# Performance work log

Hardware: AMD Instinct MI355X
Metric: run time of the kernel (lower is better)

Reference implementation:

```python
import jax, jax.numpy as jnp
import numpy as np

N = 65536      # batch of CPU-state samples
D = 64         # byte-embedding dim
H = 512        # expert hidden dim
V = 256        # byte vocabulary / result logits
NFLAGS = 8
# number of embedded inputs per expert
KS = {"alu": 4, "logic": 4, "move": 5, "flow": 6, "stack": 6}


def setup_inputs() -> dict:
    key = jax.random.key(0)
    ks = list(jax.random.split(key, 64))
    nk = lambda: ks.pop()
    rint = lambda mx: jax.random.randint(nk(), (N,), 0, mx, dtype=jnp.int32)
    inp = {n: rint(256) for n in ["A", "X", "Y", "SP", "P", "PCH", "PCL", "Op", "Val"]}
    # deterministic opcode -> functional-unit map (stand-in for build_fu_map)
    inp["fu_map"] = (jnp.arange(256, dtype=jnp.int32) % 5)
    p = lambda shape: jax.random.normal(nk(), shape, dtype=jnp.float32) * 0.02
    for name, k in KS.items():
        inp[f"{name}_emb"] = p((k, V, D))
        inp[f"{name}_W1"] = p((k * D, H))
        inp[f"{name}_b1"] = jnp.zeros((H,), jnp.float32)
    inp["alu_Wr"] = p((H, V)); inp["alu_Wf"] = p((H, NFLAGS))
    inp["logic_Wr"] = p((H, V)); inp["logic_Wf"] = p((H, NFLAGS))
    inp["move_Wo"] = p((H, V))
    inp["flow_Wo"] = p((H, V))
    inp["stack_Wo"] = p((H, V))
    return inp


def _expert_hidden(emb, idx_list, W1, b1):
    # emb: [k, 256, D]; idx_list: k arrays of [N] byte indices
    ids = jnp.stack(idx_list)                                  # [k, N]
    f = emb[jnp.arange(emb.shape[0])[:, None], ids]            # [k, N, D] gather
    f = jnp.moveaxis(f, 0, 1).reshape(ids.shape[1], -1)        # [N, k*D]
    return jax.nn.gelu(f @ W1 + b1)                            # [N, H]


def reference(A, X, Y, SP, P, PCH, PCL, Op, Val, fu_map,
              alu_emb, alu_W1, alu_b1, alu_Wr, alu_Wf,
              logic_emb, logic_W1, logic_b1, logic_Wr, logic_Wf,
              move_emb, move_W1, move_b1, move_Wo,
              flow_emb, flow_W1, flow_b1, flow_Wo,
              stack_emb, stack_W1, stack_b1, stack_Wo):
    # deterministic zero-cost router: opcode -> FU id
    fu = fu_map[Op]                                            # [N]
    carry = P & 1                                              # carry bit of status reg
    mask = lambda k: (fu == k)[:, None].astype(jnp.float32)
    # ALU (FU 0): a, operand, carry, opcode -> result + flags logits
    h = _expert_hidden(alu_emb, [A, Val, carry, Op], alu_W1, alu_b1)
    alu = jnp.concatenate([h @ alu_Wr, h @ alu_Wf], -1) * mask(0)      # [N, 264]
    # LOGIC (FU 1): same inputs, separate params
    h = _expert_hidden(logic_emb, [A, Val, carry, Op], logic_W1, logic_b1)
    logic = jnp.concatenate([h @ logic_Wr, h @ logic_Wf], -1) * mask(1)  # [N, 264]
    # MOVE (FU 2): a, x, y, operand, opcode
    move = (_expert_hidden(move_emb, [A, X, Y, Val, Op], move_W1, move_b1) @ move_Wo) * mask(2)
    # FLOW (FU 3): pc (as PCH,PCL bytes), flags, target, sp, opcode
    flow = (_expert_hidden(flow_emb, [PCH, PCL, P, Val, SP, Op], flow_W1, flow_b1) @ flow_Wo) * mask(3)
    # STACK (FU 4): a, x, sp, flags, stack_top, opcode
    stack = (_expert_hidden(stack_emb, [A, X, SP, P, Val, Op], stack_W1, stack_b1) @ stack_Wo) * mask(4)
    # dense capacity-1 dispatch: each sample's row is nonzero only in its FU's slice
    return jnp.concatenate([alu, logic, move, flow, stack], -1)        # [N, 1296]
```

## Files before the change

kernel.cpp:

```cpp
#include <hip/hip_runtime.h>

#define DEV __device__ __forceinline__

typedef __attribute__((ext_vector_type(8))) short short8;
typedef __attribute__((ext_vector_type(4))) float f32x4;
typedef unsigned short u16;

struct Ptrs { const void* p[32]; };

constexpr int N_TOK = 65536;
constexpr int cK  [5] = {4,4,5,6,6};
constexpr int cK1 [5] = {256,256,320,384,384};
constexpr int cKT [5] = {8,8,10,12,12};
constexpr int cN2 [5] = {264,264,256,256,256};
constexpr int cNT [5] = {17,17,16,16,16};
constexpr int cC0 [5] = {0,264,528,784,1040};
constexpr int cKID[5][6] = {{0,8,9,7,0,0},{0,8,9,7,0,0},{0,1,2,8,7,0},
                            {5,6,4,8,3,7},{0,1,3,4,8,7}};
constexpr int cEOFF[5] = {0,65536,131072,212992,311296};
constexpr int cWOFF[5] = {0,131072,262144,425984,622592};
constexpr int cHOFF[5] = {0,139264,278528,417792,557056};
constexpr int EMB_TOT = 409600, W1_TOT = 819200, HEAD_TOT = 696320;
constexpr int PREP_TOT = EMB_TOT + W1_TOT + HEAD_TOT;

constexpr size_t WS_COUNTS = 0;
constexpr size_t WS_BUCKET = 256;
constexpr size_t WS_EMB    = 256 + (size_t)5 * N_TOK * 4;
constexpr size_t WS_W1T    = WS_EMB + (size_t)EMB_TOT * 2;
constexpr size_t WS_HT     = WS_W1T + (size_t)W1_TOT * 2;

constexpr int ROWS = 64;
constexpr int HP   = 520;

struct Smem {
  u16 hbuf[ROWS * HP];
  int tokb[ROWS];
  int idsb[ROWS * 6];
};

DEV u16 f2bf(float f) {
  unsigned u = __builtin_bit_cast(unsigned, f);
  u += 0x7FFFu + ((u >> 16) & 1u);
  return (u16)(u >> 16);
}

DEV float gelu_f(float x) {
  float u = 0.7978845608028654f * x * (1.0f + 0.044715f * x * x);
  float t2 = fminf(fmaxf(2.0f * u, -30.0f), 30.0f);
  float e = __expf(t2);
  float th = (e - 1.0f) / (e + 1.0f);
  return 0.5f * x * (1.0f + th);
}

__global__ __launch_bounds__(256) void prep_kernel(Ptrs in, u16* embB, u16* w1tB, u16* hTB) {
  int idx = blockIdx.x * 256 + threadIdx.x;
  if (idx < EMB_TOT) {
    int e = 0, off = idx;
    while (off >= cK[e] * 16384) { off -= cK[e] * 16384; ++e; }
    const float* src = (const float*)in.p[10 + 3*e];
    embB[cEOFF[e] + off] = f2bf(src[off]);
  } else if (idx < EMB_TOT + W1_TOT) {
    int off = idx - EMB_TOT;
    int e = 0;
    while (off >= 512 * cK1[e]) { off -= 512 * cK1[e]; ++e; }
    int K1 = cK1[e];
    int n = off / K1, k = off - n * K1;
    const float* w1 = (const float*)in.p[11 + 3*e];
    w1tB[cWOFF[e] + off] = f2bf(w1[k * 512 + n]);
  } else {
    int off = idx - (EMB_TOT + W1_TOT);
    int e = off / 139264, r = off - e * 139264;
    int n = r >> 9, k = r & 511;
    float v = 0.0f;
    if (e < 2) {
      if (n < 256)       v = ((const float*)in.p[25 + 2*e])[k * 256 + n];
      else if (n < 264)  v = ((const float*)in.p[26 + 2*e])[k * 8 + (n - 256)];
    } else {
      if (n < 256)       v = ((const float*)in.p[29 + (e - 2)])[k * 256 + n];
    }
    hTB[cHOFF[e] + r] = f2bf(v);
  }
}

__global__ __launch_bounds__(256) void bucket_kernel(const int* Op, const int* fu_map,
                                                     int* counts, int* buckets) {
  __shared__ int lc[5], lb[5];
  int tid = threadIdx.x;
  if (tid < 5) lc[tid] = 0;
  __syncthreads();
  int t = blockIdx.x * 256 + tid;
  int fu = fu_map[Op[t]];
  int lp = atomicAdd(&lc[fu], 1);
  __syncthreads();
  if (tid < 5) lb[tid] = atomicAdd(&counts[tid], lc[tid]);
  __syncthreads();
  buckets[fu * N_TOK + lb[fu] + lp] = t;
}

template<int E>
DEV void expert_tile(const Ptrs& in, int tile, int count, const int* buckets,
                     const u16* embB, const u16* w1tB, const u16* hTB,
                     float* out, Smem& sm) {
  constexpr int K1 = cK1[E], KT = cKT[E], N2 = cN2[E], C0 = cC0[E];
  constexpr int NT = cNT[E], KE = cK[E];

  const int tid = threadIdx.x;
  const int vr = min(count - tile * ROWS, ROWS);
  const int rbase = E * N_TOK + tile * ROWS;

  __syncthreads();

  if (tid < ROWS)
    sm.tokb[tid] = (tid < vr) ? buckets[rbase + tid] : -1;
  for (int i = tid; i < ROWS * KE; i += 256) {
    int r = i / KE, k = i - r * KE;
    int t = buckets[rbase + ((r < vr) ? r : 0)];
    int s = cKID[E][k];
    int v = (s == 9) ? (((const int*)in.p[4])[t] & 1)
                     : ((const int*)in.p[s])[t];
    sm.idsb[r * 6 + k] = v;
  }
  __syncthreads();

  const int lane = tid & 63, wave = tid >> 6;
  const int l15 = lane & 15, lq = lane >> 4;

  {
    constexpr int ZC  = (1296 - N2) / 4;
    constexpr int ZLO = C0 / 4;
    constexpr int ZHI = (C0 + N2) / 4;
    const f32x4 z4 = {0.f, 0.f, 0.f, 0.f};
    for (int r = wave; r < vr; r += 4) {
      float* rowp = out + (size_t)sm.tokb[r] * 1296;
      #pragma unroll
      for (int c = 0; c < ZC; c += 64) {
        int cc = c + lane;
        if (cc < ZC) {
          int col4 = (cc < ZLO) ? cc : (cc - ZLO + ZHI);
          __builtin_nontemporal_store(z4, (f32x4*)(rowp + col4 * 4));
        }
      }
    }
  }

  int myids[4][KE];
  #pragma unroll
  for (int m = 0; m < 4; ++m)
    #pragma unroll
    for (int k = 0; k < KE; ++k)
      myids[m][k] = sm.idsb[(m * 16 + l15) * 6 + k];

  const u16* embE = embB + cEOFF[E];
  const u16* w1e  = w1tB + cWOFF[E];
  const float* b1 = (const float*)in.p[12 + 3 * E];

  #pragma unroll 1
  for (int half = 0; half < 2; ++half) {
    f32x4 acc[4][4];
    const f32x4 z = {0.f, 0.f, 0.f, 0.f};
    #pragma unroll
    for (int m = 0; m < 4; ++m)
      #pragma unroll
      for (int nt = 0; nt < 4; ++nt) acc[m][nt] = z;

    #pragma unroll
    for (int kt = 0; kt < KT; ++kt) {
      const int kf = kt >> 1;
      const int d  = (kt & 1) * 32 + lq * 8;
      short8 a[4];
      #pragma unroll
      for (int m = 0; m < 4; ++m)
        a[m] = *(const short8*)(embE + ((size_t)(kf * 256 + myids[m][kf]) << 6) + d);
      #pragma unroll
      for (int nt = 0; nt < 4; ++nt) {
        int n0 = wave * 128 + half * 64 + nt * 16;
        short8 b = *(const short8*)(w1e + (n0 + l15) * K1 + kt * 32 + lq * 8);
        #pragma unroll
        for (int m = 0; m < 4; ++m)
          acc[m][nt] = __builtin_amdgcn_mfma_f32_16x16x32_bf16(a[m], b, acc[m][nt], 0, 0, 0);
      }
    }
    #pragma unroll
    for (int nt = 0; nt < 4; ++nt) {
      int col = wave * 128 + half * 64 + nt * 16 + l15;
      float b1v = b1[col];
      #pragma unroll
      for (int m = 0; m < 4; ++m)
        #pragma unroll
        for (int r = 0; r < 4; ++r)
          sm.hbuf[(m * 16 + lq * 4 + r) * HP + col] = f2bf(gelu_f(acc[m][nt][r] + b1v));
    }
  }
  __syncthreads();

  const u16* hTe = hTB + cHOFF[E];
  f32x4 acc2[4][5];
  {
    const f32x4 z = {0.f, 0.f, 0.f, 0.f};
    #pragma unroll
    for (int m = 0; m < 4; ++m)
      #pragma unroll
      for (int j = 0; j < 5; ++j) acc2[m][j] = z;
  }
  #pragma unroll 4
  for (int kt = 0; kt < 16; ++kt) {
    short8 a[4];
    #pragma unroll
    for (int m = 0; m < 4; ++m)
      a[m] = *(const short8*)(sm.hbuf + (m * 16 + l15) * HP + kt * 32 + lq * 8);
    #pragma unroll
    for (int j = 0; j < 5; ++j) {
      int nt = wave + 4 * j;
      if (nt >= NT) break;
      short8 b = *(const short8*)(hTe + (nt * 16 + l15) * 512 + kt * 32 + lq * 8);
      #pragma unroll
      for (int m = 0; m < 4; ++m)
        acc2[m][j] = __builtin_amdgcn_mfma_f32_16x16x32_bf16(a[m], b, acc2[m][j], 0, 0, 0);
    }
  }

  int trow[4][4];
  #pragma unroll
  for (int m = 0; m < 4; ++m)
    #pragma unroll
    for (int r = 0; r < 4; ++r)
      trow[m][r] = sm.tokb[m * 16 + lq * 4 + r];

  #pragma unroll
  for (int j = 0; j < 5; ++j) {
    int nt = wave + 4 * j;
    if (nt >= NT) break;
    int coln = nt * 16 + l15;
    if (coln < N2) {
      #pragma unroll
      for (int m = 0; m < 4; ++m)
        #pragma unroll
        for (int r = 0; r < 4; ++r) {
          int t = trow[m][r];
          if (t >= 0)
            __builtin_nontemporal_store(acc2[m][j][r],
                                        out + (size_t)t * 1296 + C0 + coln);
        }
    }
  }
}

__global__ __launch_bounds__(256, 2) void moe_kernel(Ptrs in, const int* counts,
                                                     const int* buckets,
                                                     const u16* embB, const u16* w1tB,
                                                     const u16* hTB, float* out) {
  __shared__ Smem sm;
  int c0 = counts[0], c1 = counts[1], c2 = counts[2], c3 = counts[3], c4 = counts[4];
  int t0 = (c0 + ROWS - 1) / ROWS;
  int t1 = (c1 + ROWS - 1) / ROWS;
  int t2 = (c2 + ROWS - 1) / ROWS;
  int t3 = (c3 + ROWS - 1) / ROWS;
  int t4 = (c4 + ROWS - 1) / ROWS;
  int p1 = t0, p2 = p1 + t1, p3 = p2 + t2, p4 = p3 + t3, p5 = p4 + t4;

  const int x = blockIdx.x & 7;
  const int slot = blockIdx.x >> 3;
  const int beg = (x * p5) >> 3;
  const int end = ((x + 1) * p5) >> 3;

  for (int g = beg + slot; g < end; g += 64) {
    int e = 0, base = 0, cnt = c0;
    if (g >= p1) { e = 1; base = p1; cnt = c1; }
    if (g >= p2) { e = 2; base = p2; cnt = c2; }
    if (g >= p3) { e = 3; base = p3; cnt = c3; }
    if (g >= p4) { e = 4; base = p4; cnt = c4; }
    int tile = g - base;
    switch (e) {
      case 0: expert_tile<0>(in, tile, cnt, buckets, embB, w1tB, hTB, out, sm); break;
      case 1: expert_tile<1>(in, tile, cnt, buckets, embB, w1tB, hTB, out, sm); break;
      case 2: expert_tile<2>(in, tile, cnt, buckets, embB, w1tB, hTB, out, sm); break;
      case 3: expert_tile<3>(in, tile, cnt, buckets, embB, w1tB, hTB, out, sm); break;
      case 4: expert_tile<4>(in, tile, cnt, buckets, embB, w1tB, hTB, out, sm); break;
    }
  }
}

extern "C" void kernel_launch(void* const* d_in, const int* in_sizes, int n_in,
                              void* d_out, int out_size, void* d_ws, size_t ws_size,
                              hipStream_t stream) {
  char* ws = (char*)d_ws;
  int* counts  = (int*)(ws + WS_COUNTS);
  int* buckets = (int*)(ws + WS_BUCKET);
  u16* embB    = (u16*)(ws + WS_EMB);
  u16* w1tB    = (u16*)(ws + WS_W1T);
  u16* hTB     = (u16*)(ws + WS_HT);

  Ptrs P;
  for (int i = 0; i < 32; ++i) P.p[i] = d_in[i];

  (void)hipMemsetAsync(counts, 0, 5 * sizeof(int), stream);
  prep_kernel<<<PREP_TOT / 256, 256, 0, stream>>>(P, embB, w1tB, hTB);
  bucket_kernel<<<N_TOK / 256, 256, 0, stream>>>((const int*)d_in[7], (const int*)d_in[9],
                                                 counts, buckets);
  moe_kernel<<<512, 256, 0, stream>>>(P, counts, buckets, embB, w1tB, hTB,
                                      (float*)d_out);
}
```

Measured before the change: 282.4 us.

## Double row tile to 128 and stage gathered embeddings in swizzled LDS

Each tile now covers 128 token rows with 512 threads (8 waves) instead of 64 rows with 256. The embedding rows are gathered once into LDS with an XOR swizzle before the first GEMM, rather than each wave re-fetching them from global memory per k-step. Each wave now owns 64 hidden columns across all 128 rows, so every W1 and head weight fragment is reused over twice as many rows. In exchange it needs about 137 KB of dynamic shared memory, which likely limits each CU to one block and may require a raised dynamic-LDS limit. It also raises accumulator register pressure.

```diff
diff --git a/kernel.cpp b/kernel.cpp
--- a/kernel.cpp
+++ b/kernel.cpp
@@ -11,7 +11,6 @@
 constexpr int N_TOK = 65536;
 constexpr int cK  [5] = {4,4,5,6,6};
 constexpr int cK1 [5] = {256,256,320,384,384};
-constexpr int cKT [5] = {8,8,10,12,12};
 constexpr int cN2 [5] = {264,264,256,256,256};
 constexpr int cNT [5] = {17,17,16,16,16};
 constexpr int cC0 [5] = {0,264,528,784,1040};
@@ -29,14 +28,12 @@
 constexpr size_t WS_W1T    = WS_EMB + (size_t)EMB_TOT * 2;
 constexpr size_t WS_HT     = WS_W1T + (size_t)W1_TOT * 2;
 
-constexpr int ROWS = 64;
+constexpr int ROWS = 128;
 constexpr int HP   = 520;
 
-struct Smem {
-  u16 hbuf[ROWS * HP];
-  int tokb[ROWS];
-  int idsb[ROWS * 6];
-};
+constexpr int TOK_OFF = ROWS * HP * 2;
+constexpr int IDS_OFF = TOK_OFF + ROWS * 4;
+constexpr int LDS_BYTES = IDS_OFF + ROWS * 6 * 4;
 
 DEV u16 f2bf(float f) {
   unsigned u = __builtin_bit_cast(unsigned, f);
@@ -100,9 +97,15 @@
 template<int E>
 DEV void expert_tile(const Ptrs& in, int tile, int count, const int* buckets,
                      const u16* embB, const u16* w1tB, const u16* hTB,
-                     float* out, Smem& sm) {
-  constexpr int K1 = cK1[E], KT = cKT[E], N2 = cN2[E], C0 = cC0[E];
+                     float* out, char* smem) {
+  constexpr int K1 = cK1[E], KT = cK1[E] / 32, N2 = cN2[E], C0 = cC0[E];
   constexpr int NT = cNT[E], KE = cK[E];
+  constexpr int FB  = K1 * 2;
+  constexpr int CPR = KE * 8;
+
+  u16* hbuf = (u16*)smem;
+  int* tokb = (int*)(smem + TOK_OFF);
+  int* idsb = (int*)(smem + IDS_OFF);
 
   const int tid = threadIdx.x;
   const int vr = min(count - tile * ROWS, ROWS);
@@ -111,27 +114,27 @@
   __syncthreads();
 
   if (tid < ROWS)
-    sm.tokb[tid] = (tid < vr) ? buckets[rbase + tid] : -1;
-  for (int i = tid; i < ROWS * KE; i += 256) {
+    tokb[tid] = (tid < vr) ? buckets[rbase + tid] : -1;
+  for (int i = tid; i < ROWS * KE; i += 512) {
     int r = i / KE, k = i - r * KE;
     int t = buckets[rbase + ((r < vr) ? r : 0)];
     int s = cKID[E][k];
     int v = (s == 9) ? (((const int*)in.p[4])[t] & 1)
                      : ((const int*)in.p[s])[t];
-    sm.idsb[r * 6 + k] = v;
+    idsb[r * 6 + k] = v;
   }
   __syncthreads();
 
   const int lane = tid & 63, wave = tid >> 6;
-  const int l15 = lane & 15, lq = lane >> 4;
+  const int l15 = lane & 15, lq = (lane >> 4) & 3;
 
   {
     constexpr int ZC  = (1296 - N2) / 4;
     constexpr int ZLO = C0 / 4;
     constexpr int ZHI = (C0 + N2) / 4;
     const f32x4 z4 = {0.f, 0.f, 0.f, 0.f};
-    for (int r = wave; r < vr; r += 4) {
-      float* rowp = out + (size_t)sm.tokb[r] * 1296;
+    for (int r = wave; r < vr; r += 8) {
+      float* rowp = out + (size_t)tokb[r] * 1296;
       #pragma unroll
       for (int c = 0; c < ZC; c += 64) {
         int cc = c + lane;
@@ -143,113 +146,124 @@
     }
   }
 
-  int myids[4][KE];
-  #pragma unroll
-  for (int m = 0; m < 4; ++m)
-    #pragma unroll
-    for (int k = 0; k < KE; ++k)
-      myids[m][k] = sm.idsb[(m * 16 + l15) * 6 + k];
-
-  const u16* embE = embB + cEOFF[E];
+  {
+    const u16* embE = embB + cEOFF[E];
+    short8 val[KT];
+    int    dst[KT];
+    #pragma unroll
+    for (int it = 0; it < KT; ++it) {
+      int d = tid + it * 512;
+      int r = d / CPR, c = d - r * CPR;
+      int k = c >> 3;
+      int id = idsb[r * 6 + k];
+      val[it] = *(const short8*)(embE + (size_t)((k * 256 + id) << 6) + ((c & 7) << 3));
+      dst[it] = r * FB + ((c * 16) ^ ((r & 7) << 4));
+    }
+    #pragma unroll
+    for (int it = 0; it < KT; ++it)
+      *(short8*)(smem + dst[it]) = val[it];
+  }
+  __syncthreads();
+
   const u16* w1e  = w1tB + cWOFF[E];
   const float* b1 = (const float*)in.p[12 + 3 * E];
 
-  #pragma unroll 1
-  for (int half = 0; half < 2; ++half) {
-    f32x4 acc[4][4];
-    const f32x4 z = {0.f, 0.f, 0.f, 0.f};
-    #pragma unroll
-    for (int m = 0; m < 4; ++m)
-      #pragma unroll
-      for (int nt = 0; nt < 4; ++nt) acc[m][nt] = z;
-
-    #pragma unroll
-    for (int kt = 0; kt < KT; ++kt) {
-      const int kf = kt >> 1;
-      const int d  = (kt & 1) * 32 + lq * 8;
-      short8 a[4];
-      #pragma unroll
-      for (int m = 0; m < 4; ++m)
-        a[m] = *(const short8*)(embE + ((size_t)(kf * 256 + myids[m][kf]) << 6) + d);
-      #pragma unroll
-      for (int nt = 0; nt < 4; ++nt) {
-        int n0 = wave * 128 + half * 64 + nt * 16;
-        short8 b = *(const short8*)(w1e + (n0 + l15) * K1 + kt * 32 + lq * 8);
-        #pragma unroll
-        for (int m = 0; m < 4; ++m)
-          acc[m][nt] = __builtin_amdgcn_mfma_f32_16x16x32_bf16(a[m], b, acc[m][nt], 0, 0, 0);
-      }
-    }
-    #pragma unroll
-    for (int nt = 0; nt < 4; ++nt) {
-      int col = wave * 128 + half * 64 + nt * 16 + l15;
-      float b1v = b1[col];
-      #pragma unroll
-      for (int m = 0; m < 4; ++m)
-        #pragma unroll
-        for (int r = 0; r < 4; ++r)
-          sm.hbuf[(m * 16 + lq * 4 + r) * HP + col] = f2bf(gelu_f(acc[m][nt][r] + b1v));
-    }
-  }
-  __syncthreads();
-
-  const u16* hTe = hTB + cHOFF[E];
-  f32x4 acc2[4][5];
+  f32x4 acc[8][4];
   {
     const f32x4 z = {0.f, 0.f, 0.f, 0.f};
     #pragma unroll
-    for (int m = 0; m < 4; ++m)
-      #pragma unroll
-      for (int j = 0; j < 5; ++j) acc2[m][j] = z;
+    for (int m = 0; m < 8; ++m)
+      #pragma unroll
+      for (int nt = 0; nt < 4; ++nt) acc[m][nt] = z;
+  }
+  #pragma unroll 2
+  for (int kt = 0; kt < KT; ++kt) {
+    short8 a[8], b[4];
+    #pragma unroll
+    for (int m = 0; m < 8; ++m) {
+      int row = m * 16 + l15;
+      a[m] = *(const short8*)(smem + row * FB + ((kt * 64 + lq * 16) ^ ((row & 7) << 4)));
+    }
+    #pragma unroll
+    for (int nt = 0; nt < 4; ++nt)
+      b[nt] = *(const short8*)(w1e + (wave * 64 + nt * 16 + l15) * K1 + kt * 32 + lq * 8);
+    #pragma unroll
+    for (int nt = 0; nt < 4; ++nt)
+      #pragma unroll
+      for (int m = 0; m < 8; ++m)
+        acc[m][nt] = __builtin_amdgcn_mfma_f32_16x16x32_bf16(a[m], b[nt], acc[m][nt], 0, 0, 0);
+  }
+  __syncthreads();
+
+  #pragma unroll
+  for (int nt = 0; nt < 4; ++nt) {
+    int col = wave * 64 + nt * 16 + l15;
+    float b1v = b1[col];
+    #pragma unroll
+    for (int m = 0; m < 8; ++m)
+      #pragma unroll
+      for (int q = 0; q < 4; ++q)
+        hbuf[(m * 16 + lq * 4 + q) * HP + col] = f2bf(gelu_f(acc[m][nt][q] + b1v));
+  }
+  __syncthreads();
+
+  const u16* hTe = hTB + cHOFF[E];
+  f32x4 acc2[8][3];
+  {
+    const f32x4 z = {0.f, 0.f, 0.f, 0.f};
+    #pragma unroll
+    for (int m = 0; m < 8; ++m)
+      #pragma unroll
+      for (int j = 0; j < 3; ++j) acc2[m][j] = z;
   }
   #pragma unroll 4
   for (int kt = 0; kt < 16; ++kt) {
-    short8 a[4];
-    #pragma unroll
-    for (int m = 0; m < 4; ++m)
-      a[m] = *(const short8*)(sm.hbuf + (m * 16 + l15) * HP + kt * 32 + lq * 8);
-    #pragma unroll
-    for (int j = 0; j < 5; ++j) {
-      int nt = wave + 4 * j;
+    short8 a[8];
+    #pragma unroll
+    for (int m = 0; m < 8; ++m)
+      a[m] = *(const short8*)(hbuf + (m * 16 + l15) * HP + kt * 32 + lq * 8);
+    #pragma unroll
+    for (int j = 0; j < 3; ++j) {
+      int nt = wave + 8 * j;
       if (nt >= NT) break;
       short8 b = *(const short8*)(hTe + (nt * 16 + l15) * 512 + kt * 32 + lq * 8);
       #pragma unroll
-      for (int m = 0; m < 4; ++m)
+      for (int m = 0; m < 8; ++m)
         acc2[m][j] = __builtin_amdgcn_mfma_f32_16x16x32_bf16(a[m], b, acc2[m][j], 0, 0, 0);
     }
   }
 
-  int trow[4][4];
+  int trow[8][4];
   #pragma unroll
-  for (int m = 0; m < 4; ++m)
-    #pragma unroll
-    for (int r = 0; r < 4; ++r)
-      trow[m][r] = sm.tokb[m * 16 + lq * 4 + r];
+  for (int m = 0; m < 8; ++m)
+    #pragma unroll
+    for (int q = 0; q < 4; ++q)
+      trow[m][q] = tokb[m * 16 + lq * 4 + q];
 
   #pragma unroll
-  for (int j = 0; j < 5; ++j) {
-    int nt = wave + 4 * j;
+  for (int j = 0; j < 3; ++j) {
+    int nt = wave + 8 * j;
     if (nt >= NT) break;
     int coln = nt * 16 + l15;
     if (coln < N2) {
       #pragma unroll
-      for (int m = 0; m < 4; ++m)
+      for (int m = 0; m < 8; ++m)
         #pragma unroll
-        for (int r = 0; r < 4; ++r) {
-          int t = trow[m][r];
+        for (int q = 0; q < 4; ++q) {
+          int t = trow[m][q];
           if (t >= 0)
-            __builtin_nontemporal_store(acc2[m][j][r],
+            __builtin_nontemporal_store(acc2[m][j][q],
                                         out + (size_t)t * 1296 + C0 + coln);
         }
     }
   }
 }
 
-__global__ __launch_bounds__(256, 2) void moe_kernel(Ptrs in, const int* counts,
+__global__ __launch_bounds__(512, 2) void moe_kernel(Ptrs in, const int* counts,
                                                      const int* buckets,
                                                      const u16* embB, const u16* w1tB,
                                                      const u16* hTB, float* out) {
-  __shared__ Smem sm;
+  extern __shared__ char smem[];
   int c0 = counts[0], c1 = counts[1], c2 = counts[2], c3 = counts[3], c4 = counts[4];
   int t0 = (c0 + ROWS - 1) / ROWS;
   int t1 = (c1 + ROWS - 1) / ROWS;
@@ -271,11 +285,11 @@
     if (g >= p4) { e = 4; base = p4; cnt = c4; }
     int tile = g - base;
     switch (e) {
-      case 0: expert_tile<0>(in, tile, cnt, buckets, embB, w1tB, hTB, out, sm); break;
-      case 1: expert_tile<1>(in, tile, cnt, buckets, embB, w1tB, hTB, out, sm); break;
-      case 2: expert_tile<2>(in, tile, cnt, buckets, embB, w1tB, hTB, out, sm); break;
-      case 3: expert_tile<3>(in, tile, cnt, buckets, embB, w1tB, hTB, out, sm); break;
-      case 4: expert_tile<4>(in, tile, cnt, buckets, embB, w1tB, hTB, out, sm); break;
+      case 0: expert_tile<0>(in, tile, cnt, buckets, embB, w1tB, hTB, out, smem); break;
+      case 1: expert_tile<1>(in, tile, cnt, buckets, embB, w1tB, hTB, out, smem); break;
+      case 2: expert_tile<2>(in, tile, cnt, buckets, embB, w1tB, hTB, out, smem); break;
+      case 3: expert_tile<3>(in, tile, cnt, buckets, embB, w1tB, hTB, out, smem); break;
+      case 4: expert_tile<4>(in, tile, cnt, buckets, embB, w1tB, hTB, out, smem); break;
     }
   }
 }
@@ -297,6 +311,6 @@
   prep_kernel<<<PREP_TOT / 256, 256, 0, stream>>>(P, embB, w1tB, hTB);
   bucket_kernel<<<N_TOK / 256, 256, 0, stream>>>((const int*)d_in[7], (const int*)d_in[9],
                                                  counts, buckets);
-  moe_kernel<<<512, 256, 0, stream>>>(P, counts, buckets, embB, w1tB, hTB,
-                                      (float*)d_out);
-}
+  moe_kernel<<<512, 512, LDS_BYTES, stream>>>(P, counts, buckets, embB, w1tB, hTB,
+                                              (float*)d_out);
+}
```

Result: faster. 236.5 us (-16.2%).

## Double-buffer MFMA operand loads and stage output through LDS for coalesced stores

Applied to the files above, without the earlier changes.

Adds register double-buffering for the embedding and W1 operand loads in the first GEMM, and for the head-weight loads in the second GEMM, so that global loads for step k+1 overlap MFMAs for step k. The fp32 results are written to an LDS staging buffer (reusing the hidden buffer region) and then stored with coalesced 16-byte nontemporal writes per row, replacing scattered scalar stores. The grid doubles to 1024 blocks, the slot stride changes to match, and the second launch-bounds argument is dropped. This raises register pressure and adds two barriers, and occupancy may drop.

```diff
diff --git a/kernel.cpp b/kernel.cpp
--- a/kernel.cpp
+++ b/kernel.cpp
@@ -11,7 +11,6 @@
 constexpr int N_TOK = 65536;
 constexpr int cK  [5] = {4,4,5,6,6};
 constexpr int cK1 [5] = {256,256,320,384,384};
-constexpr int cKT [5] = {8,8,10,12,12};
 constexpr int cN2 [5] = {264,264,256,256,256};
 constexpr int cNT [5] = {17,17,16,16,16};
 constexpr int cC0 [5] = {0,264,528,784,1040};
@@ -31,12 +30,13 @@
 
 constexpr int ROWS = 64;
 constexpr int HP   = 520;
-
-struct Smem {
-  u16 hbuf[ROWS * HP];
-  int tokb[ROWS];
-  int idsb[ROWS * 6];
-};
+constexpr int RP   = 268;
+
+constexpr int TOK_OFF = 0;
+constexpr int IDS_OFF = 256;
+constexpr int BUF_OFF = 2048;
+constexpr int BUF_SZ  = ROWS * RP * 4;
+constexpr int LDS_BYTES = BUF_OFF + BUF_SZ;
 
 DEV u16 f2bf(float f) {
   unsigned u = __builtin_bit_cast(unsigned, f);
@@ -100,9 +100,14 @@
 template<int E>
 DEV void expert_tile(const Ptrs& in, int tile, int count, const int* buckets,
                      const u16* embB, const u16* w1tB, const u16* hTB,
-                     float* out, Smem& sm) {
-  constexpr int K1 = cK1[E], KT = cKT[E], N2 = cN2[E], C0 = cC0[E];
+                     float* out, char* smem) {
+  constexpr int K1 = cK1[E], KT = cK1[E] / 32, N2 = cN2[E], C0 = cC0[E];
   constexpr int NT = cNT[E], KE = cK[E];
+
+  u16*   hbuf = (u16*)(smem + BUF_OFF);
+  float* rbuf = (float*)(smem + BUF_OFF);
+  int*   tokb = (int*)(smem + TOK_OFF);
+  int*   idsb = (int*)(smem + IDS_OFF);
 
   const int tid = threadIdx.x;
   const int vr = min(count - tile * ROWS, ROWS);
@@ -111,27 +116,27 @@
   __syncthreads();
 
   if (tid < ROWS)
-    sm.tokb[tid] = (tid < vr) ? buckets[rbase + tid] : -1;
+    tokb[tid] = (tid < vr) ? buckets[rbase + tid] : -1;
   for (int i = tid; i < ROWS * KE; i += 256) {
     int r = i / KE, k = i - r * KE;
     int t = buckets[rbase + ((r < vr) ? r : 0)];
     int s = cKID[E][k];
     int v = (s == 9) ? (((const int*)in.p[4])[t] & 1)
                      : ((const int*)in.p[s])[t];
-    sm.idsb[r * 6 + k] = v;
+    idsb[r * 6 + k] = v;
   }
   __syncthreads();
 
   const int lane = tid & 63, wave = tid >> 6;
-  const int l15 = lane & 15, lq = lane >> 4;
+  const int l15 = lane & 15, lq = (lane >> 4) & 3;
 
   {
-    constexpr int ZC  = (1296 - N2) / 4;
     constexpr int ZLO = C0 / 4;
     constexpr int ZHI = (C0 + N2) / 4;
+    constexpr int ZC  = 324 - (N2 / 4);
     const f32x4 z4 = {0.f, 0.f, 0.f, 0.f};
     for (int r = wave; r < vr; r += 4) {
-      float* rowp = out + (size_t)sm.tokb[r] * 1296;
+      float* rowp = out + (size_t)tokb[r] * 1296;
       #pragma unroll
       for (int c = 0; c < ZC; c += 64) {
         int cc = c + lane;
@@ -148,7 +153,7 @@
   for (int m = 0; m < 4; ++m)
     #pragma unroll
     for (int k = 0; k < KE; ++k)
-      myids[m][k] = sm.idsb[(m * 16 + l15) * 6 + k];
+      myids[m][k] = idsb[(m * 16 + l15) * 6 + k];
 
   const u16* embE = embB + cEOFF[E];
   const u16* w1e  = w1tB + cWOFF[E];
@@ -163,32 +168,44 @@
       #pragma unroll
       for (int nt = 0; nt < 4; ++nt) acc[m][nt] = z;
 
+    const int n0b = wave * 128 + half * 64;
+    short8 aa[2][4], bb[2][4];
+    #pragma unroll
+    for (int m = 0; m < 4; ++m)
+      aa[0][m] = *(const short8*)(embE + ((size_t)myids[m][0] << 6) + lq * 8);
+    #pragma unroll
+    for (int nt = 0; nt < 4; ++nt)
+      bb[0][nt] = *(const short8*)(w1e + (n0b + nt * 16 + l15) * K1 + lq * 8);
+
     #pragma unroll
     for (int kt = 0; kt < KT; ++kt) {
-      const int kf = kt >> 1;
-      const int d  = (kt & 1) * 32 + lq * 8;
-      short8 a[4];
+      const int cur = kt & 1, nxt = cur ^ 1;
+      if (kt + 1 < KT) {
+        const int kf = (kt + 1) >> 1;
+        const int d  = ((kt + 1) & 1) * 32 + lq * 8;
+        #pragma unroll
+        for (int m = 0; m < 4; ++m)
+          aa[nxt][m] = *(const short8*)(embE + ((size_t)(kf * 256 + myids[m][kf]) << 6) + d);
+        #pragma unroll
+        for (int nt = 0; nt < 4; ++nt)
+          bb[nxt][nt] = *(const short8*)(w1e + (n0b + nt * 16 + l15) * K1 + (kt + 1) * 32 + lq * 8);
+      }
+      #pragma unroll
+      for (int nt = 0; nt < 4; ++nt)
+        #pragma unroll
+        for (int m = 0; m < 4; ++m)
+          acc[m][nt] = __builtin_amdgcn_mfma_f32_16x16x32_bf16(aa[cur][m], bb[cur][nt], acc[m][nt], 0, 0, 0);
+    }
+
+    #pragma unroll
+    for (int nt = 0; nt < 4; ++nt) {
+      int col = n0b + nt * 16 + l15;
+      float b1v = b1[col];
       #pragma unroll
       for (int m = 0; m < 4; ++m)
-        a[m] = *(const short8*)(embE + ((size_t)(kf * 256 + myids[m][kf]) << 6) + d);
-      #pragma unroll
-      for (int nt = 0; nt < 4; ++nt) {
-        int n0 = wave * 128 + half * 64 + nt * 16;
-        short8 b = *(const short8*)(w1e + (n0 + l15) * K1 + kt * 32 + lq * 8);
-        #pragma unroll
-        for (int m = 0; m < 4; ++m)
-          acc[m][nt] = __builtin_amdgcn_mfma_f32_16x16x32_bf16(a[m], b, acc[m][nt], 0, 0, 0);
-      }
-    }
-    #pragma unroll
-    for (int nt = 0; nt < 4; ++nt) {
-      int col = wave * 128 + half * 64 + nt * 16 + l15;
-      float b1v = b1[col];
-      #pragma unroll
-      for (int m = 0; m < 4; ++m)
-        #pragma unroll
-        for (int r = 0; r < 4; ++r)
-          sm.hbuf[(m * 16 + lq * 4 + r) * HP + col] = f2bf(gelu_f(acc[m][nt][r] + b1v));
+        #pragma unroll
+        for (int q = 0; q < 4; ++q)
+          hbuf[(m * 16 + lq * 4 + q) * HP + col] = f2bf(gelu_f(acc[m][nt][q] + b1v));
     }
   }
   __syncthreads();
@@ -202,54 +219,80 @@
       #pragma unroll
       for (int j = 0; j < 5; ++j) acc2[m][j] = z;
   }
-  #pragma unroll 4
-  for (int kt = 0; kt < 16; ++kt) {
-    short8 a[4];
-    #pragma unroll
-    for (int m = 0; m < 4; ++m)
-      a[m] = *(const short8*)(sm.hbuf + (m * 16 + l15) * HP + kt * 32 + lq * 8);
+  {
+    short8 b2[2][5];
     #pragma unroll
     for (int j = 0; j < 5; ++j) {
       int nt = wave + 4 * j;
-      if (nt >= NT) break;
-      short8 b = *(const short8*)(hTe + (nt * 16 + l15) * 512 + kt * 32 + lq * 8);
+      if (nt < NT)
+        b2[0][j] = *(const short8*)(hTe + (nt * 16 + l15) * 512 + lq * 8);
+    }
+    #pragma unroll
+    for (int kt = 0; kt < 16; ++kt) {
+      const int cur = kt & 1, nxt = cur ^ 1;
+      if (kt < 15) {
+        #pragma unroll
+        for (int j = 0; j < 5; ++j) {
+          int nt = wave + 4 * j;
+          if (nt < NT)
+            b2[nxt][j] = *(const short8*)(hTe + (nt * 16 + l15) * 512 + (kt + 1) * 32 + lq * 8);
+        }
+      }
+      short8 a[4];
       #pragma unroll
       for (int m = 0; m < 4; ++m)
-        acc2[m][j] = __builtin_amdgcn_mfma_f32_16x16x32_bf16(a[m], b, acc2[m][j], 0, 0, 0);
-    }
-  }
-
-  int trow[4][4];
-  #pragma unroll
-  for (int m = 0; m < 4; ++m)
-    #pragma unroll
-    for (int r = 0; r < 4; ++r)
-      trow[m][r] = sm.tokb[m * 16 + lq * 4 + r];
+        a[m] = *(const short8*)(hbuf + (m * 16 + l15) * HP + kt * 32 + lq * 8);
+      #pragma unroll
+      for (int j = 0; j < 5; ++j) {
+        int nt = wave + 4 * j;
+        if (nt < NT)
+          #pragma unroll
+          for (int m = 0; m < 4; ++m)
+            acc2[m][j] = __builtin_amdgcn_mfma_f32_16x16x32_bf16(a[m], b2[cur][j], acc2[m][j], 0, 0, 0);
+      }
+    }
+  }
+  __syncthreads();
 
   #pragma unroll
   for (int j = 0; j < 5; ++j) {
     int nt = wave + 4 * j;
-    if (nt >= NT) break;
-    int coln = nt * 16 + l15;
-    if (coln < N2) {
-      #pragma unroll
-      for (int m = 0; m < 4; ++m)
-        #pragma unroll
-        for (int r = 0; r < 4; ++r) {
-          int t = trow[m][r];
-          if (t >= 0)
-            __builtin_nontemporal_store(acc2[m][j][r],
-                                        out + (size_t)t * 1296 + C0 + coln);
+    if (nt < NT) {
+      int coln = nt * 16 + l15;
+      if (coln < N2) {
+        #pragma unroll
+        for (int m = 0; m < 4; ++m)
+          #pragma unroll
+          for (int q = 0; q < 4; ++q)
+            rbuf[(m * 16 + lq * 4 + q) * RP + coln] = acc2[m][j][q];
+      }
+    }
+  }
+  __syncthreads();
+
+  {
+    constexpr int V = N2 / 4;
+    for (int r = wave; r < vr; r += 4) {
+      int t = tokb[r];
+      float* dst = out + (size_t)t * 1296 + C0;
+      const float* src = rbuf + r * RP;
+      #pragma unroll
+      for (int c = 0; c < V; c += 64) {
+        int cc = c + lane;
+        if (cc < V) {
+          f32x4 v = *(const f32x4*)(src + cc * 4);
+          __builtin_nontemporal_store(v, (f32x4*)(dst + cc * 4));
         }
-    }
-  }
-}
-
-__global__ __launch_bounds__(256, 2) void moe_kernel(Ptrs in, const int* counts,
-                                                     const int* buckets,
-                                                     const u16* embB, const u16* w1tB,
-                                                     const u16* hTB, float* out) {
-  __shared__ Smem sm;
+      }
+    }
+  }
+}
+
+__global__ __launch_bounds__(256) void moe_kernel(Ptrs in, const int* counts,
+                                                  const int* buckets,
+                                                  const u16* embB, const u16* w1tB,
+                                                  const u16* hTB, float* out) {
+  extern __shared__ char smem[];
   int c0 = counts[0], c1 = counts[1], c2 = counts[2], c3 = counts[3], c4 = counts[4];
   int t0 = (c0 + ROWS - 1) / ROWS;
   int t1 = (c1 + ROWS - 1) / ROWS;
@@ -263,7 +306,7 @@
   const int beg = (x * p5) >> 3;
   const int end = ((x + 1) * p5) >> 3;
 
-  for (int g = beg + slot; g < end; g += 64) {
+  for (int g = beg + slot; g < end; g += 128) {
     int e = 0, base = 0, cnt = c0;
     if (g >= p1) { e = 1; base = p1; cnt = c1; }
     if (g >= p2) { e = 2; base = p2; cnt = c2; }
@@ -271,11 +314,11 @@
     if (g >= p4) { e = 4; base = p4; cnt = c4; }
     int tile = g - base;
     switch (e) {
-      case 0: expert_tile<0>(in, tile, cnt, buckets, embB, w1tB, hTB, out, sm); break;
-      case 1: expert_tile<1>(in, tile, cnt, buckets, embB, w1tB, hTB, out, sm); break;
-      case 2: expert_tile<2>(in, tile, cnt, buckets, embB, w1tB, hTB, out, sm); break;
-      case 3: expert_tile<3>(in, tile, cnt, buckets, embB, w1tB, hTB, out, sm); break;
-      case 4: expert_tile<4>(in, tile, cnt, buckets, embB, w1tB, hTB, out, sm); break;
+      case 0: expert_tile<0>(in, tile, cnt, buckets, embB, w1tB, hTB, out, smem); break;
+      case 1: expert_tile<1>(in, tile, cnt, buckets, embB, w1tB, hTB, out, smem); break;
+      case 2: expert_tile<2>(in, tile, cnt, buckets, embB, w1tB, hTB, out, smem); break;
+      case 3: expert_tile<3>(in, tile, cnt, buckets, embB, w1tB, hTB, out, smem); break;
+      case 4: expert_tile<4>(in, tile, cnt, buckets, embB, w1tB, hTB, out, smem); break;
     }
   }
 }
@@ -297,6 +340,6 @@
   prep_kernel<<<PREP_TOT / 256, 256, 0, stream>>>(P, embB, w1tB, hTB);
   bucket_kernel<<<N_TOK / 256, 256, 0, stream>>>((const int*)d_in[7], (const int*)d_in[9],
                                                  counts, buckets);
-  moe_kernel<<<512, 256, 0, stream>>>(P, counts, buckets, embB, w1tB, hTB,
-                                      (float*)d_out);
-}
+  moe_kernel<<<1024, 256, LDS_BYTES, stream>>>(P, counts, buckets, embB, w1tB, hTB,
+                                               (float*)d_out);
+}
```

After: 336.3 us. 1.19x slower.

## Write expert outputs to compact buffer, then expand rows with a separate kernel

Applied to the files above, without the earlier changes.

The MoE kernel now stages each tile's head outputs in LDS and writes them contiguously into a compact workspace buffer indexed by bucket position, instead of scattering per-element stores and zero-fills into the full output. A new expand kernel reads each token's compact row and writes the entire 1296-wide output row with full-width nontemporal vector stores, zeros included. The bucket kernel records each token's position for this lookup. This trades scattered, partial-row writes for coalesced ones, at the cost of an extra kernel launch and an extra write and read of the compact intermediate.

```diff
diff --git a/kernel.cpp b/kernel.cpp
--- a/kernel.cpp
+++ b/kernel.cpp
@@ -11,7 +11,6 @@
 constexpr int N_TOK = 65536;
 constexpr int cK  [5] = {4,4,5,6,6};
 constexpr int cK1 [5] = {256,256,320,384,384};
-constexpr int cKT [5] = {8,8,10,12,12};
 constexpr int cN2 [5] = {264,264,256,256,256};
 constexpr int cNT [5] = {17,17,16,16,16};
 constexpr int cC0 [5] = {0,264,528,784,1040};
@@ -28,15 +27,17 @@
 constexpr size_t WS_EMB    = 256 + (size_t)5 * N_TOK * 4;
 constexpr size_t WS_W1T    = WS_EMB + (size_t)EMB_TOT * 2;
 constexpr size_t WS_HT     = WS_W1T + (size_t)W1_TOT * 2;
+constexpr size_t WS_POS    = WS_HT + (size_t)HEAD_TOT * 2;
+constexpr size_t WS_COMP   = WS_POS + (size_t)N_TOK * 4;
 
 constexpr int ROWS = 64;
 constexpr int HP   = 520;
-
-struct Smem {
-  u16 hbuf[ROWS * HP];
-  int tokb[ROWS];
-  int idsb[ROWS * 6];
-};
+constexpr int RP   = 272;
+
+constexpr int IDS_OFF = 0;
+constexpr int BUF_OFF = 2048;
+constexpr int BUF_SZ  = ROWS * RP * 4;
+constexpr int LDS_BYTES = BUF_OFF + BUF_SZ;
 
 DEV u16 f2bf(float f) {
   unsigned u = __builtin_bit_cast(unsigned, f);
@@ -83,7 +84,7 @@
 }
 
 __global__ __launch_bounds__(256) void bucket_kernel(const int* Op, const int* fu_map,
-                                                     int* counts, int* buckets) {
+                                                     int* counts, int* buckets, int* posOf) {
   __shared__ int lc[5], lb[5];
   int tid = threadIdx.x;
   if (tid < 5) lc[tid] = 0;
@@ -94,15 +95,21 @@
   __syncthreads();
   if (tid < 5) lb[tid] = atomicAdd(&counts[tid], lc[tid]);
   __syncthreads();
-  buckets[fu * N_TOK + lb[fu] + lp] = t;
+  int pos = lb[fu] + lp;
+  buckets[fu * N_TOK + pos] = t;
+  posOf[t] = pos;
 }
 
 template<int E>
-DEV void expert_tile(const Ptrs& in, int tile, int count, const int* buckets,
+DEV void expert_tile(const Ptrs& in, int tile, int count, int gbase, const int* buckets,
                      const u16* embB, const u16* w1tB, const u16* hTB,
-                     float* out, Smem& sm) {
-  constexpr int K1 = cK1[E], KT = cKT[E], N2 = cN2[E], C0 = cC0[E];
+                     float* comp, char* smem) {
+  constexpr int K1 = cK1[E], KT = cK1[E] / 32, N2 = cN2[E];
   constexpr int NT = cNT[E], KE = cK[E];
+
+  u16*   hbuf = (u16*)(smem + BUF_OFF);
+  float* rbuf = (float*)(smem + BUF_OFF);
+  int*   idsb = (int*)(smem + IDS_OFF);
 
   const int tid = threadIdx.x;
   const int vr = min(count - tile * ROWS, ROWS);
@@ -110,45 +117,25 @@
 
   __syncthreads();
 
-  if (tid < ROWS)
-    sm.tokb[tid] = (tid < vr) ? buckets[rbase + tid] : -1;
   for (int i = tid; i < ROWS * KE; i += 256) {
     int r = i / KE, k = i - r * KE;
     int t = buckets[rbase + ((r < vr) ? r : 0)];
     int s = cKID[E][k];
     int v = (s == 9) ? (((const int*)in.p[4])[t] & 1)
                      : ((const int*)in.p[s])[t];
-    sm.idsb[r * 6 + k] = v;
+    idsb[r * 6 + k] = v;
   }
   __syncthreads();
 
   const int lane = tid & 63, wave = tid >> 6;
-  const int l15 = lane & 15, lq = lane >> 4;
-
-  {
-    constexpr int ZC  = (1296 - N2) / 4;
-    constexpr int ZLO = C0 / 4;
-    constexpr int ZHI = (C0 + N2) / 4;
-    const f32x4 z4 = {0.f, 0.f, 0.f, 0.f};
-    for (int r = wave; r < vr; r += 4) {
-      float* rowp = out + (size_t)sm.tokb[r] * 1296;
-      #pragma unroll
-      for (int c = 0; c < ZC; c += 64) {
-        int cc = c + lane;
-        if (cc < ZC) {
-          int col4 = (cc < ZLO) ? cc : (cc - ZLO + ZHI);
-          __builtin_nontemporal_store(z4, (f32x4*)(rowp + col4 * 4));
-        }
-      }
-    }
-  }
+  const int l15 = lane & 15, lq = (lane >> 4) & 3;
 
   int myids[4][KE];
   #pragma unroll
   for (int m = 0; m < 4; ++m)
     #pragma unroll
     for (int k = 0; k < KE; ++k)
-      myids[m][k] = sm.idsb[(m * 16 + l15) * 6 + k];
+      myids[m][k] = idsb[(m * 16 + l15) * 6 + k];
 
   const u16* embE = embB + cEOFF[E];
   const u16* w1e  = w1tB + cWOFF[E];
@@ -163,32 +150,33 @@
       #pragma unroll
       for (int nt = 0; nt < 4; ++nt) acc[m][nt] = z;
 
+    const int n0b = wave * 128 + half * 64;
     #pragma unroll
     for (int kt = 0; kt < KT; ++kt) {
       const int kf = kt >> 1;
       const int d  = (kt & 1) * 32 + lq * 8;
-      short8 a[4];
+      short8 a[4], b[4];
       #pragma unroll
       for (int m = 0; m < 4; ++m)
         a[m] = *(const short8*)(embE + ((size_t)(kf * 256 + myids[m][kf]) << 6) + d);
       #pragma unroll
-      for (int nt = 0; nt < 4; ++nt) {
-        int n0 = wave * 128 + half * 64 + nt * 16;
-        short8 b = *(const short8*)(w1e + (n0 + l15) * K1 + kt * 32 + lq * 8);
+      for (int nt = 0; nt < 4; ++nt)
+        b[nt] = *(const short8*)(w1e + (n0b + nt * 16 + l15) * K1 + kt * 32 + lq * 8);
+      #pragma unroll
+      for (int nt = 0; nt < 4; ++nt)
         #pragma unroll
         for (int m = 0; m < 4; ++m)
-          acc[m][nt] = __builtin_amdgcn_mfma_f32_16x16x32_bf16(a[m], b, acc[m][nt], 0, 0, 0);
-      }
+          acc[m][nt] = __builtin_amdgcn_mfma_f32_16x16x32_bf16(a[m], b[nt], acc[m][nt], 0, 0, 0);
     }
     #pragma unroll
     for (int nt = 0; nt < 4; ++nt) {
-      int col = wave * 128 + half * 64 + nt * 16 + l15;
+      int col = n0b + nt * 16 + l15;
       float b1v = b1[col];
       #pragma unroll
       for (int m = 0; m < 4; ++m)
         #pragma unroll
-        for (int r = 0; r < 4; ++r)
-          sm.hbuf[(m * 16 + lq * 4 + r) * HP + col] = f2bf(gelu_f(acc[m][nt][r] + b1v));
+        for (int q = 0; q < 4; ++q)
+          hbuf[(m * 16 + lq * 4 + q) * HP + col] = f2bf(gelu_f(acc[m][nt][q] + b1v));
     }
   }
   __syncthreads();
@@ -207,7 +195,7 @@
     short8 a[4];
     #pragma unroll
     for (int m = 0; m < 4; ++m)
-      a[m] = *(const short8*)(sm.hbuf + (m * 16 + l15) * HP + kt * 32 + lq * 8);
+      a[m] = *(const short8*)(hbuf + (m * 16 + l15) * HP + kt * 32 + lq * 8);
     #pragma unroll
     for (int j = 0; j < 5; ++j) {
       int nt = wave + 4 * j;
@@ -218,13 +206,7 @@
         acc2[m][j] = __builtin_amdgcn_mfma_f32_16x16x32_bf16(a[m], b, acc2[m][j], 0, 0, 0);
     }
   }
-
-  int trow[4][4];
-  #pragma unroll
-  for (int m = 0; m < 4; ++m)
-    #pragma unroll
-    for (int r = 0; r < 4; ++r)
-      trow[m][r] = sm.tokb[m * 16 + lq * 4 + r];
+  __syncthreads();
 
   #pragma unroll
   for (int j = 0; j < 5; ++j) {
@@ -235,21 +217,25 @@
       #pragma unroll
       for (int m = 0; m < 4; ++m)
         #pragma unroll
-        for (int r = 0; r < 4; ++r) {
-          int t = trow[m][r];
-          if (t >= 0)
-            __builtin_nontemporal_store(acc2[m][j][r],
-                                        out + (size_t)t * 1296 + C0 + coln);
-        }
-    }
+        for (int q = 0; q < 4; ++q)
+          rbuf[(m * 16 + lq * 4 + q) * RP + coln] = acc2[m][j][q];
+    }
+  }
+  __syncthreads();
+
+  {
+    float* dstc = comp + (size_t)(gbase + tile * ROWS) * RP;
+    const int tot = vr * (RP / 4);
+    for (int idx = tid; idx < tot; idx += 256)
+      *(f32x4*)(dstc + idx * 4) = *(const f32x4*)(rbuf + idx * 4);
   }
 }
 
 __global__ __launch_bounds__(256, 2) void moe_kernel(Ptrs in, const int* counts,
                                                      const int* buckets,
                                                      const u16* embB, const u16* w1tB,
-                                                     const u16* hTB, float* out) {
-  __shared__ Smem sm;
+                                                     const u16* hTB, float* comp) {
+  extern __shared__ char smem[];
   int c0 = counts[0], c1 = counts[1], c2 = counts[2], c3 = counts[3], c4 = counts[4];
   int t0 = (c0 + ROWS - 1) / ROWS;
   int t1 = (c1 + ROWS - 1) / ROWS;
@@ -257,6 +243,7 @@
   int t3 = (c3 + ROWS - 1) / ROWS;
   int t4 = (c4 + ROWS - 1) / ROWS;
   int p1 = t0, p2 = p1 + t1, p3 = p2 + t2, p4 = p3 + t3, p5 = p4 + t4;
+  int b1 = c0, b2 = b1 + c1, b3 = b2 + c2, b4 = b3 + c3;
 
   const int x = blockIdx.x & 7;
   const int slot = blockIdx.x >> 3;
@@ -264,18 +251,45 @@
   const int end = ((x + 1) * p5) >> 3;
 
   for (int g = beg + slot; g < end; g += 64) {
-    int e = 0, base = 0, cnt = c0;
-    if (g >= p1) { e = 1; base = p1; cnt = c1; }
-    if (g >= p2) { e = 2; base = p2; cnt = c2; }
-    if (g >= p3) { e = 3; base = p3; cnt = c3; }
-    if (g >= p4) { e = 4; base = p4; cnt = c4; }
+    int e = 0, base = 0, cnt = c0, gb = 0;
+    if (g >= p1) { e = 1; base = p1; cnt = c1; gb = b1; }
+    if (g >= p2) { e = 2; base = p2; cnt = c2; gb = b2; }
+    if (g >= p3) { e = 3; base = p3; cnt = c3; gb = b3; }
+    if (g >= p4) { e = 4; base = p4; cnt = c4; gb = b4; }
     int tile = g - base;
     switch (e) {
-      case 0: expert_tile<0>(in, tile, cnt, buckets, embB, w1tB, hTB, out, sm); break;
-      case 1: expert_tile<1>(in, tile, cnt, buckets, embB, w1tB, hTB, out, sm); break;
-      case 2: expert_tile<2>(in, tile, cnt, buckets, embB, w1tB, hTB, out, sm); break;
-      case 3: expert_tile<3>(in, tile, cnt, buckets, embB, w1tB, hTB, out, sm); break;
-      case 4: expert_tile<4>(in, tile, cnt, buckets, embB, w1tB, hTB, out, sm); break;
+      case 0: expert_tile<0>(in, tile, cnt, gb, buckets, embB, w1tB, hTB, comp, smem); break;
+      case 1: expert_tile<1>(in, tile, cnt, gb, buckets, embB, w1tB, hTB, comp, smem); break;
+      case 2: expert_tile<2>(in, tile, cnt, gb, buckets, embB, w1tB, hTB, comp, smem); break;
+      case 3: expert_tile<3>(in, tile, cnt, gb, buckets, embB, w1tB, hTB, comp, smem); break;
+      case 4: expert_tile<4>(in, tile, cnt, gb, buckets, embB, w1tB, hTB, comp, smem); break;
+    }
+  }
+}
+
+__global__ __launch_bounds__(256) void expand_kernel(const int* Op, const int* fu_map,
+                                                     const int* counts, const int* posOf,
+                                                     const float* comp, float* out) {
+  int b[5];
+  b[0] = 0; b[1] = counts[0]; b[2] = b[1] + counts[1];
+  b[3] = b[2] + counts[2]; b[4] = b[3] + counts[3];
+  const int lane = threadIdx.x & 63, wv = threadIdx.x >> 6;
+  for (int t = blockIdx.x * 4 + wv; t < N_TOK; t += gridDim.x * 4) {
+    int fu = fu_map[Op[t]];
+    int slot = b[fu] + posOf[t];
+    int c0q = cC0[fu] >> 2;
+    int n2q = cN2[fu] >> 2;
+    const float* cr = comp + (size_t)slot * RP;
+    float* orow = out + (size_t)t * 1296;
+    #pragma unroll
+    for (int it = 0; it < 6; ++it) {
+      int c4 = it * 64 + lane;
+      if (c4 < 324) {
+        f32x4 v = {0.f, 0.f, 0.f, 0.f};
+        int rel = c4 - c0q;
+        if (rel >= 0 && rel < n2q) v = *(const f32x4*)(cr + rel * 4);
+        __builtin_nontemporal_store(v, (f32x4*)(orow + c4 * 4));
+      }
     }
   }
 }
@@ -289,6 +303,8 @@
   u16* embB    = (u16*)(ws + WS_EMB);
   u16* w1tB    = (u16*)(ws + WS_W1T);
   u16* hTB     = (u16*)(ws + WS_HT);
+  int* posOf   = (int*)(ws + WS_POS);
+  float* comp  = (float*)(ws + WS_COMP);
 
   Ptrs P;
   for (int i = 0; i < 32; ++i) P.p[i] = d_in[i];
@@ -296,7 +312,8 @@
   (void)hipMemsetAsync(counts, 0, 5 * sizeof(int), stream);
   prep_kernel<<<PREP_TOT / 256, 256, 0, stream>>>(P, embB, w1tB, hTB);
   bucket_kernel<<<N_TOK / 256, 256, 0, stream>>>((const int*)d_in[7], (const int*)d_in[9],
-                                                 counts, buckets);
-  moe_kernel<<<512, 256, 0, stream>>>(P, counts, buckets, embB, w1tB, hTB,
-                                      (float*)d_out);
-}
+                                                 counts, buckets, posOf);
+  moe_kernel<<<512, 256, LDS_BYTES, stream>>>(P, counts, buckets, embB, w1tB, hTB, comp);
+  expand_kernel<<<2048, 256, 0, stream>>>((const int*)d_in[7], (const int*)d_in[9],
+                                          counts, posOf, comp, (float*)d_out);
+}
```

Result: faster. 275.4 us (-2.5%).
